# Kernel tuning notes

Measured on AMD Instinct MI355X. Metric: run time of the kernel, lower is better.

Reference implementation:

```python
import jax, jax.numpy as jnp
import numpy as np

N = 500000   # active voxels
CIN = 32
COUT = 64
K = 27       # 3x3x3 kernel taps
G = 8        # group norm groups
EPS = 1e-5


def group_norm(x, gamma, beta, num_groups=G, eps=EPS):
    # fvnn GroupNorm on sparse features with batch size 1: normalize each
    # channel-group over all active voxels (spatial) and channels in group.
    n, c = x.shape
    xg = x.reshape(n, num_groups, c // num_groups)
    mean = xg.mean(axis=(0, 2), keepdims=True)
    var = xg.var(axis=(0, 2), keepdims=True)
    xn = ((xg - mean) * jax.lax.rsqrt(var + eps)).reshape(n, c)
    return xn * gamma + beta


def sparse_conv(x, nbr_idx, W):
    # gather-based sparse 3x3x3 conv: W is [K, Cin, Cout]; loop over the 27
    # fixed kernel taps to avoid materializing the full [N, K, Cin] gather.
    out = jnp.zeros((x.shape[0], W.shape[2]), x.dtype)
    for k in range(W.shape[0]):
        out = out + jnp.take(x, nbr_idx[:, k], axis=0) @ W[k]
    return out


def setup_inputs() -> dict:
    key = jax.random.key(0)
    ks = jax.random.split(key, 8)
    s1 = 1.0 / np.sqrt(K * CIN)
    s2 = 1.0 / np.sqrt(K * COUT)
    return {
        "x": jax.random.normal(ks[0], (N, CIN), jnp.float32),
        "nbr_idx": jax.random.randint(ks[1], (N, K), 0, N, jnp.int32),
        "gamma1": jnp.ones((CIN,), jnp.float32),
        "beta1": jnp.zeros((CIN,), jnp.float32),
        "W1": jax.random.normal(ks[2], (K, CIN, COUT), jnp.float32) * s1,
        "gamma2": jnp.ones((COUT,), jnp.float32),
        "beta2": jnp.zeros((COUT,), jnp.float32),
        "W2": jax.random.normal(ks[3], (K, COUT, COUT), jnp.float32) * s2,
        "Wskip": jax.random.normal(ks[4], (CIN, COUT), jnp.float32) * (1.0 / np.sqrt(CIN)),
        "bskip": jnp.zeros((COUT,), jnp.float32),
        "feat_depth": 0,
    }


def reference(x, nbr_idx, gamma1, beta1, W1, gamma2, beta2, W2, Wskip, bskip, feat_depth):
    # decoder SparseResBlock, order 'gcs': GN -> SparseConv(bias=False) -> SiLU
    h = jax.nn.silu(sparse_conv(group_norm(x, gamma1, beta1), nbr_idx, W1))
    h = jax.nn.silu(sparse_conv(group_norm(h, gamma2, beta2), nbr_idx, W2))
    skip = x @ Wskip + bskip  # 1x1 sparse conv == per-voxel linear
    return (h + skip, feat_depth)
```

## Files before the change

kernel.cpp:

```cpp
#include <hip/hip_runtime.h>
#include <hip/hip_bf16.h>

typedef __bf16 bf16x8 __attribute__((ext_vector_type(8)));
typedef __bf16 bf16x4 __attribute__((ext_vector_type(4)));
typedef float  f32x4  __attribute__((ext_vector_type(4)));

#define MFMA16(a, b, c) __builtin_amdgcn_mfma_f32_16x16x32_bf16((a), (b), (c), 0, 0, 0)

__global__ void zero_stats_kernel(float* s) { s[threadIdx.x] = 0.0f; }

__global__ __launch_bounds__(256) void caststats_kernel(
    const float4* __restrict__ x, bf16x4* __restrict__ xb,
    float* __restrict__ stats, int nvec)
{
    int nth = gridDim.x * blockDim.x;
    int gt = blockIdx.x * blockDim.x + threadIdx.x;
    float s = 0.f, ss = 0.f;
    for (int f = gt; f < nvec; f += nth) {
        float4 v = x[f];
        s  += v.x + v.y + v.z + v.w;
        ss += v.x * v.x + v.y * v.y + v.z * v.z + v.w * v.w;
        bf16x4 b;
        b[0] = (__bf16)v.x; b[1] = (__bf16)v.y;
        b[2] = (__bf16)v.z; b[3] = (__bf16)v.w;
        xb[f] = b;
    }
    __shared__ float ls[16];
    if (threadIdx.x < 16) ls[threadIdx.x] = 0.f;
    __syncthreads();
    int g = gt & 7;
    atomicAdd(&ls[2 * g], s);
    atomicAdd(&ls[2 * g + 1], ss);
    __syncthreads();
    if (threadIdx.x < 16) atomicAdd(&stats[threadIdx.x], ls[threadIdx.x]);
}

__global__ __launch_bounds__(256) void fold1_kernel(
    const float* __restrict__ W1, const float* __restrict__ gamma1,
    const float* __restrict__ beta1, const float* __restrict__ Wskip,
    const float* __restrict__ stats1,
    __bf16* __restrict__ bp1, __bf16* __restrict__ bps,
    float* __restrict__ bias1,
    const int* __restrict__ feat, int* __restrict__ feat_out, float inv_n)
{
    int b = blockIdx.x, t = threadIdx.x;
    if (b < 216) {
        int e = b * 256 + t;
        int j = e & 7, lane = (e >> 3) & 63, ct = (e >> 9) & 3, k = e >> 11;
        int ci = ((lane >> 4) << 3) + j;
        int co = (ct << 4) + (lane & 15);
        int g = ci >> 2;
        float mean = stats1[2 * g] * inv_n;
        float var  = stats1[2 * g + 1] * inv_n - mean * mean;
        float r = rsqrtf(var + 1e-5f);
        float a = gamma1[ci] * r;
        bp1[e] = (__bf16)(a * W1[k * 2048 + ci * 64 + co]);
    } else if (b == 216) {
        if (t < 64) {
            float sum = 0.0f;
            for (int ci = 0; ci < 32; ++ci) {
                int g = ci >> 2;
                float mean = stats1[2 * g] * inv_n;
                float var  = stats1[2 * g + 1] * inv_n - mean * mean;
                float r = rsqrtf(var + 1e-5f);
                float a = gamma1[ci] * r;
                float bb = beta1[ci] - mean * a;
                float ws = 0.0f;
                for (int k = 0; k < 27; ++k) ws += W1[k * 2048 + ci * 64 + t];
                sum += bb * ws;
            }
            bias1[t] = sum;
        } else if (t == 64) {
            feat_out[0] = feat[0];
        }
    } else {
        int e = (b - 217) * 256 + t;
        int j = e & 7, lane = (e >> 3) & 63, ct = e >> 9;
        int ci = ((lane >> 4) << 3) + j;
        int co = (ct << 4) + (lane & 15);
        bps[e] = (__bf16)Wskip[ci * 64 + co];
    }
}

__global__ __launch_bounds__(256) void fold2_kernel(
    const float* __restrict__ W2, const float* __restrict__ gamma2,
    const float* __restrict__ beta2, const float* __restrict__ stats2,
    __bf16* __restrict__ bp2, float* __restrict__ bias2, float inv_n)
{
    int b = blockIdx.x, t = threadIdx.x;
    if (b < 432) {
        int e = b * 256 + t;
        int j = e & 7, lane = (e >> 3) & 63, ct = (e >> 9) & 3, hf = (e >> 11) & 1, k = e >> 12;
        int ci = (hf << 5) + ((lane >> 4) << 3) + j;
        int co = (ct << 4) + (lane & 15);
        int g = ci >> 3;
        float mean = stats2[2 * g] * inv_n;
        float var  = stats2[2 * g + 1] * inv_n - mean * mean;
        float r = rsqrtf(var + 1e-5f);
        float a = gamma2[ci] * r;
        bp2[e] = (__bf16)(a * W2[k * 4096 + ci * 64 + co]);
    } else if (t < 64) {
        float sum = 0.0f;
        for (int ci = 0; ci < 64; ++ci) {
            int g = ci >> 3;
            float mean = stats2[2 * g] * inv_n;
            float var  = stats2[2 * g + 1] * inv_n - mean * mean;
            float r = rsqrtf(var + 1e-5f);
            float a = gamma2[ci] * r;
            float bb = beta2[ci] - mean * a;
            float ws = 0.0f;
            for (int k = 0; k < 27; ++k) ws += W2[k * 4096 + ci * 64 + t];
            sum += bb * ws;
        }
        bias2[t] = sum;
    }
}

__global__ __launch_bounds__(256, 4) void conv1_kernel(
    const __bf16* __restrict__ xb, const int* __restrict__ nbr,
    const __bf16* __restrict__ bp1, const float* __restrict__ bias1,
    __bf16* __restrict__ h, float* __restrict__ stats2, int nTiles)
{
    __shared__ int sidx[4][864];
    __shared__ float ls[16];
    const int wav = threadIdx.x >> 6, lane = threadIdx.x & 63;
    const int unit = blockIdx.x * 4 + wav;
    const int t0 = unit * 2;
    const bool act0 = t0 < nTiles, act1 = t0 + 1 < nTiles;
    if (threadIdx.x < 16) ls[threadIdx.x] = 0.f;
    const int lm = lane & 15, q = lane >> 4;
    f32x4 c[8] = {};
    if (act0) {
        const int* gi = nbr + (size_t)t0 * 432;
        const int cnt = act1 ? 864 : 432;
        for (int i = lane; i < 864; i += 64) sidx[wav][i] = (i < cnt) ? gi[i] : 0;
        const int* s0p = &sidx[wav][lm * 27];
        const int* s1p = &sidx[wav][432 + lm * 27];
        const bf16x8* __restrict__ bpv = (const bf16x8*)bp1;
        bf16x8 a0 = *(const bf16x8*)(xb + (size_t)s0p[0] * 32 + q * 8);
        bf16x8 a1 = *(const bf16x8*)(xb + (size_t)s1p[0] * 32 + q * 8);
#pragma unroll
        for (int k = 0; k < 27; ++k) {
            bf16x8 n0 = a0, n1 = a1;
            if (k < 26) {
                n0 = *(const bf16x8*)(xb + (size_t)s0p[k + 1] * 32 + q * 8);
                n1 = *(const bf16x8*)(xb + (size_t)s1p[k + 1] * 32 + q * 8);
            }
            int bb = k * 256 + lane;
            bf16x8 b0 = bpv[bb], b1 = bpv[bb + 64], b2 = bpv[bb + 128], b3 = bpv[bb + 192];
            c[0] = MFMA16(a0, b0, c[0]);
            c[1] = MFMA16(a0, b1, c[1]);
            c[2] = MFMA16(a0, b2, c[2]);
            c[3] = MFMA16(a0, b3, c[3]);
            c[4] = MFMA16(a1, b0, c[4]);
            c[5] = MFMA16(a1, b1, c[5]);
            c[6] = MFMA16(a1, b2, c[6]);
            c[7] = MFMA16(a1, b3, c[7]);
            a0 = n0; a1 = n1;
        }
    }
    __syncthreads();
    if (act0) {
#define EPI1(CI, CT, V0) { \
        float bsv = bias1[(CT) * 16 + lm]; \
        float ps = 0.f, pss = 0.f; \
        _Pragma("unroll") \
        for (int r = 0; r < 4; ++r) { \
            float val = c[CI][r] + bsv; \
            val = val / (1.0f + __expf(-val)); \
            h[(size_t)((V0) + q * 4 + r) * 64 + (CT) * 16 + lm] = (__bf16)val; \
            ps += val; pss += val * val; } \
        int g2 = (CT) * 2 + (lm >> 3); \
        atomicAdd(&ls[2 * g2], ps); atomicAdd(&ls[2 * g2 + 1], pss); }
        const int v0 = t0 * 16;
        EPI1(0, 0, v0) EPI1(1, 1, v0) EPI1(2, 2, v0) EPI1(3, 3, v0)
        if (act1) {
            const int v1 = v0 + 16;
            EPI1(4, 0, v1) EPI1(5, 1, v1) EPI1(6, 2, v1) EPI1(7, 3, v1)
        }
#undef EPI1
    }
    __syncthreads();
    if (threadIdx.x < 16) atomicAdd(&stats2[threadIdx.x], ls[threadIdx.x]);
}

__global__ __launch_bounds__(256, 4) void conv2_kernel(
    const __bf16* __restrict__ h, const __bf16* __restrict__ xb,
    const int* __restrict__ nbr,
    const __bf16* __restrict__ bp2, const __bf16* __restrict__ bps,
    const float* __restrict__ bias2, const float* __restrict__ bskip,
    float* __restrict__ out, int nTiles)
{
    __shared__ int sidx[4][864];
    const int wav = threadIdx.x >> 6, lane = threadIdx.x & 63;
    const int unit = blockIdx.x * 4 + wav;
    const int t0 = unit * 2;
    const bool act0 = t0 < nTiles, act1 = t0 + 1 < nTiles;
    if (!act0) return;
    const int lm = lane & 15, q = lane >> 4;
    const int* gi = nbr + (size_t)t0 * 432;
    const int cnt = act1 ? 864 : 432;
    for (int i = lane; i < 864; i += 64) sidx[wav][i] = (i < cnt) ? gi[i] : 0;
    const int* s0p = &sidx[wav][lm * 27];
    const int* s1p = &sidx[wav][432 + lm * 27];
    const bf16x8* __restrict__ bpv = (const bf16x8*)bp2;
    const bf16x8* __restrict__ bsp = (const bf16x8*)bps;
    f32x4 c[8] = {};
    {
        const __bf16* r0 = h + (size_t)s0p[0] * 64;
        const __bf16* r1 = h + (size_t)s1p[0] * 64;
        bf16x8 a0l = *(const bf16x8*)(r0 + q * 8);
        bf16x8 a0h = *(const bf16x8*)(r0 + 32 + q * 8);
        bf16x8 a1l = *(const bf16x8*)(r1 + q * 8);
        bf16x8 a1h = *(const bf16x8*)(r1 + 32 + q * 8);
#pragma unroll
        for (int k = 0; k < 27; ++k) {
            bf16x8 n0l = a0l, n0h = a0h, n1l = a1l, n1h = a1h;
            if (k < 26) {
                const __bf16* p0 = h + (size_t)s0p[k + 1] * 64;
                const __bf16* p1 = h + (size_t)s1p[k + 1] * 64;
                n0l = *(const bf16x8*)(p0 + q * 8);
                n0h = *(const bf16x8*)(p0 + 32 + q * 8);
                n1l = *(const bf16x8*)(p1 + q * 8);
                n1h = *(const bf16x8*)(p1 + 32 + q * 8);
            }
            int bb = k * 512 + lane;
            bf16x8 b0 = bpv[bb],       b1 = bpv[bb + 64];
            bf16x8 b2 = bpv[bb + 128], b3 = bpv[bb + 192];
            c[0] = MFMA16(a0l, b0, c[0]);
            c[1] = MFMA16(a0l, b1, c[1]);
            c[2] = MFMA16(a0l, b2, c[2]);
            c[3] = MFMA16(a0l, b3, c[3]);
            c[4] = MFMA16(a1l, b0, c[4]);
            c[5] = MFMA16(a1l, b1, c[5]);
            c[6] = MFMA16(a1l, b2, c[6]);
            c[7] = MFMA16(a1l, b3, c[7]);
            bf16x8 b4 = bpv[bb + 256], b5 = bpv[bb + 320];
            bf16x8 b6 = bpv[bb + 384], b7 = bpv[bb + 448];
            c[0] = MFMA16(a0h, b4, c[0]);
            c[1] = MFMA16(a0h, b5, c[1]);
            c[2] = MFMA16(a0h, b6, c[2]);
            c[3] = MFMA16(a0h, b7, c[3]);
            c[4] = MFMA16(a1h, b4, c[4]);
            c[5] = MFMA16(a1h, b5, c[5]);
            c[6] = MFMA16(a1h, b6, c[6]);
            c[7] = MFMA16(a1h, b7, c[7]);
            a0l = n0l; a0h = n0h; a1l = n1l; a1h = n1h;
        }
    }
    f32x4 s[8] = {};
    {
        bf16x8 ax0 = *(const bf16x8*)(xb + ((size_t)t0 * 16 + lm) * 32 + q * 8);
        bf16x8 w0 = bsp[lane], w1 = bsp[64 + lane], w2 = bsp[128 + lane], w3 = bsp[192 + lane];
        s[0] = MFMA16(ax0, w0, s[0]);
        s[1] = MFMA16(ax0, w1, s[1]);
        s[2] = MFMA16(ax0, w2, s[2]);
        s[3] = MFMA16(ax0, w3, s[3]);
        if (act1) {
            bf16x8 ax1 = *(const bf16x8*)(xb + ((size_t)t0 * 16 + 16 + lm) * 32 + q * 8);
            s[4] = MFMA16(ax1, w0, s[4]);
            s[5] = MFMA16(ax1, w1, s[5]);
            s[6] = MFMA16(ax1, w2, s[6]);
            s[7] = MFMA16(ax1, w3, s[7]);
        }
    }
#define EPI2(CI, CT, V0) { \
        int co = (CT) * 16 + lm; \
        float b2v = bias2[co]; \
        float bsk = bskip[co]; \
        _Pragma("unroll") \
        for (int r = 0; r < 4; ++r) { \
            float val = c[CI][r] + b2v; \
            val = val / (1.0f + __expf(-val)); \
            val += s[CI][r] + bsk; \
            out[(size_t)((V0) + q * 4 + r) * 64 + co] = val; } }
    const int v0 = t0 * 16;
    EPI2(0, 0, v0) EPI2(1, 1, v0) EPI2(2, 2, v0) EPI2(3, 3, v0)
    if (act1) {
        const int v1 = v0 + 16;
        EPI2(4, 0, v1) EPI2(5, 1, v1) EPI2(6, 2, v1) EPI2(7, 3, v1)
    }
#undef EPI2
}

extern "C" void kernel_launch(void* const* d_in, const int* in_sizes, int n_in,
                              void* d_out, int out_size, void* d_ws, size_t ws_size,
                              hipStream_t stream)
{
    (void)n_in; (void)out_size; (void)ws_size;
    const float* x      = (const float*)d_in[0];
    const int*   nbr    = (const int*)d_in[1];
    const float* gamma1 = (const float*)d_in[2];
    const float* beta1  = (const float*)d_in[3];
    const float* W1     = (const float*)d_in[4];
    const float* gamma2 = (const float*)d_in[5];
    const float* beta2  = (const float*)d_in[6];
    const float* W2     = (const float*)d_in[7];
    const float* Wskip  = (const float*)d_in[8];
    const float* bskip  = (const float*)d_in[9];
    const int*   feat   = (const int*)d_in[10];
    const int N = in_sizes[0] / 32;

    char* ws = (char*)d_ws;
    float* stats1 = (float*)ws;
    float* stats2 = stats1 + 16;
    float* bias1  = stats1 + 32;
    float* bias2  = stats1 + 96;
    __bf16* bp1 = (__bf16*)(ws + (1 << 10));
    __bf16* bps = (__bf16*)(ws + (1 << 17));
    __bf16* bp2 = (__bf16*)(ws + 144 * 1024);
    __bf16* xb  = (__bf16*)(ws + (1 << 20));
    __bf16* h   = (__bf16*)(ws + (size_t)34 * (1 << 20));
    float* outb = (float*)d_out;

    const int nTiles = (N + 15) / 16;
    const int units = (nTiles + 1) / 2;
    const int convBlocks = (units + 3) / 4;

    hipLaunchKernelGGL(zero_stats_kernel, dim3(1), dim3(32), 0, stream, stats1);
    hipLaunchKernelGGL(caststats_kernel, dim3(2048), dim3(256), 0, stream,
                       (const float4*)x, (bf16x4*)xb, stats1, N * 8);
    hipLaunchKernelGGL(fold1_kernel, dim3(225), dim3(256), 0, stream,
                       W1, gamma1, beta1, Wskip, stats1, bp1, bps, bias1,
                       feat, (int*)(outb + (size_t)N * 64),
                       1.0f / (4.0f * (float)N));
    hipLaunchKernelGGL(conv1_kernel, dim3(convBlocks), dim3(256), 0, stream,
                       xb, nbr, bp1, bias1, h, stats2, nTiles);
    hipLaunchKernelGGL(fold2_kernel, dim3(433), dim3(256), 0, stream,
                       W2, gamma2, beta2, stats2, bp2, bias2,
                       1.0f / (8.0f * (float)N));
    hipLaunchKernelGGL(conv2_kernel, dim3(convBlocks), dim3(256), 0, stream,
                       h, xb, nbr, bp2, bps, bias2, bskip, outb, nTiles);
}
```

Before: 862.4 us.

## Stage conv weights in LDS via async global_load_lds and deepen gather prefetch

Both conv kernels now copy the weights for three taps at a time into shared memory with async global-to-LDS loads that all four waves of the block share, instead of each wave reading the weight fragments from global memory. Gather prefetch distance is raised to three taps in conv1 and two taps in conv2, held in small register rings. The aim is less redundant per-wave weight traffic through the cache. In exchange, each kernel adds a shared-memory buffer and two block barriers per three-tap chunk, which likely drain outstanding gather loads. Waves with no tile now stay alive to take part in the barriers.

After: 812.9 us. 1.06x faster.

```diff
diff --git a/kernel.cpp b/kernel.cpp
--- a/kernel.cpp
+++ b/kernel.cpp
@@ -6,6 +6,12 @@
 typedef float  f32x4  __attribute__((ext_vector_type(4)));
 
 #define MFMA16(a, b, c) __builtin_amdgcn_mfma_f32_16x16x32_bf16((a), (b), (c), 0, 0, 0)
+
+__device__ __forceinline__ void async_copy16(const void* g, void* l) {
+    __builtin_amdgcn_global_load_lds(
+        (const __attribute__((address_space(1))) void*)g,
+        (__attribute__((address_space(3))) void*)l, 16, 0, 0);
+}
 
 __global__ void zero_stats_kernel(float* s) { s[threadIdx.x] = 0.0f; }
 
@@ -122,6 +128,7 @@
     __bf16* __restrict__ h, float* __restrict__ stats2, int nTiles)
 {
     __shared__ int sidx[4][864];
+    __shared__ __align__(16) __bf16 Bs[3 * 2048];
     __shared__ float ls[16];
     const int wav = threadIdx.x >> 6, lane = threadIdx.x & 63;
     const int unit = blockIdx.x * 4 + wav;
@@ -129,37 +136,64 @@
     const bool act0 = t0 < nTiles, act1 = t0 + 1 < nTiles;
     if (threadIdx.x < 16) ls[threadIdx.x] = 0.f;
     const int lm = lane & 15, q = lane >> 4;
+
+    {
+        const int tc = act0 ? t0 : 0;
+        const int* gi = nbr + (size_t)tc * 432;
+        const int cnt = (act0 && act1) ? 864 : 432;
+        for (int i = lane; i < 864; i += 64) sidx[wav][i] = (i < cnt) ? gi[i] : 0;
+    }
+    const int* s0p = &sidx[wav][lm * 27];
+    const int* s1p = &sidx[wav][432 + lm * 27];
+
+#pragma unroll
+    for (int i = 0; i < 3; ++i) {
+        int part = wav * 3 + i;
+        async_copy16(bp1 + (size_t)part * 512 + lane * 8, &Bs[part * 512]);
+    }
+
     f32x4 c[8] = {};
-    if (act0) {
-        const int* gi = nbr + (size_t)t0 * 432;
-        const int cnt = act1 ? 864 : 432;
-        for (int i = lane; i < 864; i += 64) sidx[wav][i] = (i < cnt) ? gi[i] : 0;
-        const int* s0p = &sidx[wav][lm * 27];
-        const int* s1p = &sidx[wav][432 + lm * 27];
-        const bf16x8* __restrict__ bpv = (const bf16x8*)bp1;
-        bf16x8 a0 = *(const bf16x8*)(xb + (size_t)s0p[0] * 32 + q * 8);
-        bf16x8 a1 = *(const bf16x8*)(xb + (size_t)s1p[0] * 32 + q * 8);
-#pragma unroll
-        for (int k = 0; k < 27; ++k) {
-            bf16x8 n0 = a0, n1 = a1;
-            if (k < 26) {
-                n0 = *(const bf16x8*)(xb + (size_t)s0p[k + 1] * 32 + q * 8);
-                n1 = *(const bf16x8*)(xb + (size_t)s1p[k + 1] * 32 + q * 8);
+    bf16x8 P0[3], P1[3];
+#pragma unroll
+    for (int k = 0; k < 3; ++k) {
+        P0[k] = *(const bf16x8*)(xb + (size_t)s0p[k] * 32 + q * 8);
+        P1[k] = *(const bf16x8*)(xb + (size_t)s1p[k] * 32 + q * 8);
+    }
+    __syncthreads();
+
+    const bf16x8* Bv = (const bf16x8*)Bs;
+#pragma unroll
+    for (int k = 0; k < 27; ++k) {
+        const int sl = k % 3;
+        bf16x8 n0, n1;
+        if (k + 3 < 27) {
+            n0 = *(const bf16x8*)(xb + (size_t)s0p[k + 3] * 32 + q * 8);
+            n1 = *(const bf16x8*)(xb + (size_t)s1p[k + 3] * 32 + q * 8);
+        }
+        const int bb = sl * 256 + lane;
+        bf16x8 b0 = Bv[bb], b1 = Bv[bb + 64], b2 = Bv[bb + 128], b3 = Bv[bb + 192];
+        bf16x8 a0 = P0[sl], a1 = P1[sl];
+        c[0] = MFMA16(a0, b0, c[0]);
+        c[1] = MFMA16(a0, b1, c[1]);
+        c[2] = MFMA16(a0, b2, c[2]);
+        c[3] = MFMA16(a0, b3, c[3]);
+        c[4] = MFMA16(a1, b0, c[4]);
+        c[5] = MFMA16(a1, b1, c[5]);
+        c[6] = MFMA16(a1, b2, c[6]);
+        c[7] = MFMA16(a1, b3, c[7]);
+        if (k + 3 < 27) { P0[sl] = n0; P1[sl] = n1; }
+        if ((k % 3) == 2 && k < 26) {
+            __syncthreads();
+            const __bf16* gsrc = bp1 + (size_t)(k / 3 + 1) * 3 * 2048;
+#pragma unroll
+            for (int i = 0; i < 3; ++i) {
+                int part = wav * 3 + i;
+                async_copy16(gsrc + (size_t)part * 512 + lane * 8, &Bs[part * 512]);
             }
-            int bb = k * 256 + lane;
-            bf16x8 b0 = bpv[bb], b1 = bpv[bb + 64], b2 = bpv[bb + 128], b3 = bpv[bb + 192];
-            c[0] = MFMA16(a0, b0, c[0]);
-            c[1] = MFMA16(a0, b1, c[1]);
-            c[2] = MFMA16(a0, b2, c[2]);
-            c[3] = MFMA16(a0, b3, c[3]);
-            c[4] = MFMA16(a1, b0, c[4]);
-            c[5] = MFMA16(a1, b1, c[5]);
-            c[6] = MFMA16(a1, b2, c[6]);
-            c[7] = MFMA16(a1, b3, c[7]);
-            a0 = n0; a1 = n1;
-        }
-    }
-    __syncthreads();
+            __syncthreads();
+        }
+    }
+
     if (act0) {
 #define EPI1(CI, CT, V0) { \
         float bsv = bias1[(CT) * 16 + lm]; \
@@ -192,64 +226,93 @@
     float* __restrict__ out, int nTiles)
 {
     __shared__ int sidx[4][864];
+    __shared__ __align__(16) __bf16 Bs[3 * 4096];
     const int wav = threadIdx.x >> 6, lane = threadIdx.x & 63;
     const int unit = blockIdx.x * 4 + wav;
     const int t0 = unit * 2;
     const bool act0 = t0 < nTiles, act1 = t0 + 1 < nTiles;
-    if (!act0) return;
     const int lm = lane & 15, q = lane >> 4;
-    const int* gi = nbr + (size_t)t0 * 432;
-    const int cnt = act1 ? 864 : 432;
-    for (int i = lane; i < 864; i += 64) sidx[wav][i] = (i < cnt) ? gi[i] : 0;
+
+    {
+        const int tc = act0 ? t0 : 0;
+        const int* gi = nbr + (size_t)tc * 432;
+        const int cnt = (act0 && act1) ? 864 : 432;
+        for (int i = lane; i < 864; i += 64) sidx[wav][i] = (i < cnt) ? gi[i] : 0;
+    }
     const int* s0p = &sidx[wav][lm * 27];
     const int* s1p = &sidx[wav][432 + lm * 27];
-    const bf16x8* __restrict__ bpv = (const bf16x8*)bp2;
-    const bf16x8* __restrict__ bsp = (const bf16x8*)bps;
+
+#pragma unroll
+    for (int i = 0; i < 6; ++i) {
+        int part = wav * 6 + i;
+        async_copy16(bp2 + (size_t)part * 512 + lane * 8, &Bs[part * 512]);
+    }
+
     f32x4 c[8] = {};
-    {
-        const __bf16* r0 = h + (size_t)s0p[0] * 64;
-        const __bf16* r1 = h + (size_t)s1p[0] * 64;
-        bf16x8 a0l = *(const bf16x8*)(r0 + q * 8);
-        bf16x8 a0h = *(const bf16x8*)(r0 + 32 + q * 8);
-        bf16x8 a1l = *(const bf16x8*)(r1 + q * 8);
-        bf16x8 a1h = *(const bf16x8*)(r1 + 32 + q * 8);
-#pragma unroll
-        for (int k = 0; k < 27; ++k) {
-            bf16x8 n0l = a0l, n0h = a0h, n1l = a1l, n1h = a1h;
-            if (k < 26) {
-                const __bf16* p0 = h + (size_t)s0p[k + 1] * 64;
-                const __bf16* p1 = h + (size_t)s1p[k + 1] * 64;
-                n0l = *(const bf16x8*)(p0 + q * 8);
-                n0h = *(const bf16x8*)(p0 + 32 + q * 8);
-                n1l = *(const bf16x8*)(p1 + q * 8);
-                n1h = *(const bf16x8*)(p1 + 32 + q * 8);
+    bf16x8 P0l[2], P0h[2], P1l[2], P1h[2];
+#pragma unroll
+    for (int k = 0; k < 2; ++k) {
+        const __bf16* r0 = h + (size_t)s0p[k] * 64;
+        const __bf16* r1 = h + (size_t)s1p[k] * 64;
+        P0l[k] = *(const bf16x8*)(r0 + q * 8);
+        P0h[k] = *(const bf16x8*)(r0 + 32 + q * 8);
+        P1l[k] = *(const bf16x8*)(r1 + q * 8);
+        P1h[k] = *(const bf16x8*)(r1 + 32 + q * 8);
+    }
+    __syncthreads();
+
+    const bf16x8* Bv = (const bf16x8*)Bs;
+#pragma unroll
+    for (int k = 0; k < 27; ++k) {
+        const int sl = k & 1;
+        bf16x8 n0l, n0h, n1l, n1h;
+        if (k + 2 < 27) {
+            const __bf16* p0 = h + (size_t)s0p[k + 2] * 64;
+            const __bf16* p1 = h + (size_t)s1p[k + 2] * 64;
+            n0l = *(const bf16x8*)(p0 + q * 8);
+            n0h = *(const bf16x8*)(p0 + 32 + q * 8);
+            n1l = *(const bf16x8*)(p1 + q * 8);
+            n1h = *(const bf16x8*)(p1 + 32 + q * 8);
+        }
+        const int bb = (k % 3) * 512 + lane;
+        bf16x8 b0 = Bv[bb],       b1 = Bv[bb + 64];
+        bf16x8 b2 = Bv[bb + 128], b3 = Bv[bb + 192];
+        bf16x8 a0l = P0l[sl], a0h = P0h[sl], a1l = P1l[sl], a1h = P1h[sl];
+        c[0] = MFMA16(a0l, b0, c[0]);
+        c[1] = MFMA16(a0l, b1, c[1]);
+        c[2] = MFMA16(a0l, b2, c[2]);
+        c[3] = MFMA16(a0l, b3, c[3]);
+        c[4] = MFMA16(a1l, b0, c[4]);
+        c[5] = MFMA16(a1l, b1, c[5]);
+        c[6] = MFMA16(a1l, b2, c[6]);
+        c[7] = MFMA16(a1l, b3, c[7]);
+        bf16x8 b4 = Bv[bb + 256], b5 = Bv[bb + 320];
+        bf16x8 b6 = Bv[bb + 384], b7 = Bv[bb + 448];
+        c[0] = MFMA16(a0h, b4, c[0]);
+        c[1] = MFMA16(a0h, b5, c[1]);
+        c[2] = MFMA16(a0h, b6, c[2]);
+        c[3] = MFMA16(a0h, b7, c[3]);
+        c[4] = MFMA16(a1h, b4, c[4]);
+        c[5] = MFMA16(a1h, b5, c[5]);
+        c[6] = MFMA16(a1h, b6, c[6]);
+        c[7] = MFMA16(a1h, b7, c[7]);
+        if (k + 2 < 27) { P0l[sl] = n0l; P0h[sl] = n0h; P1l[sl] = n1l; P1h[sl] = n1h; }
+        if ((k % 3) == 2 && k < 26) {
+            __syncthreads();
+            const __bf16* gsrc = bp2 + (size_t)(k / 3 + 1) * 3 * 4096;
+#pragma unroll
+            for (int i = 0; i < 6; ++i) {
+                int part = wav * 6 + i;
+                async_copy16(gsrc + (size_t)part * 512 + lane * 8, &Bs[part * 512]);
             }
-            int bb = k * 512 + lane;
-            bf16x8 b0 = bpv[bb],       b1 = bpv[bb + 64];
-            bf16x8 b2 = bpv[bb + 128], b3 = bpv[bb + 192];
-            c[0] = MFMA16(a0l, b0, c[0]);
-            c[1] = MFMA16(a0l, b1, c[1]);
-            c[2] = MFMA16(a0l, b2, c[2]);
-            c[3] = MFMA16(a0l, b3, c[3]);
-            c[4] = MFMA16(a1l, b0, c[4]);
-            c[5] = MFMA16(a1l, b1, c[5]);
-            c[6] = MFMA16(a1l, b2, c[6]);
-            c[7] = MFMA16(a1l, b3, c[7]);
-            bf16x8 b4 = bpv[bb + 256], b5 = bpv[bb + 320];
-            bf16x8 b6 = bpv[bb + 384], b7 = bpv[bb + 448];
-            c[0] = MFMA16(a0h, b4, c[0]);
-            c[1] = MFMA16(a0h, b5, c[1]);
-            c[2] = MFMA16(a0h, b6, c[2]);
-            c[3] = MFMA16(a0h, b7, c[3]);
-            c[4] = MFMA16(a1h, b4, c[4]);
-            c[5] = MFMA16(a1h, b5, c[5]);
-            c[6] = MFMA16(a1h, b6, c[6]);
-            c[7] = MFMA16(a1h, b7, c[7]);
-            a0l = n0l; a0h = n0h; a1l = n1l; a1h = n1h;
-        }
-    }
+            __syncthreads();
+        }
+    }
+
+    if (!act0) return;
     f32x4 s[8] = {};
     {
+        const bf16x8* bsp = (const bf16x8*)bps;
         bf16x8 ax0 = *(const bf16x8*)(xb + ((size_t)t0 * 16 + lm) * 32 + q * 8);
         bf16x8 w0 = bsp[lane], w1 = bsp[64 + lane], w2 = bsp[128 + lane], w3 = bsp[192 + lane];
         s[0] = MFMA16(ax0, w0, s[0]);
```

## Stage conv weights in LDS via async copies and deepen gather prefetch

Applied to the files above, without the earlier changes.

Both sparse conv kernels now stream the folded weight chunks (three taps at a time) into double-buffered shared memory using global_load_lds async copies, synchronised with barriers and explicit waitcnts. The neighbor-row gathers are prefetched six taps ahead in registers instead of one. The aim is to stop each wave reloading weights from global/L2 every tap and to hide gather latency better. In exchange, conv2 drops to 2 blocks per CU, more registers are live, inactive waves must stay alive for the barriers, and block-wide barriers per chunk add sync cost.

Result: slower. 1.657 ms (+92.2%).

```diff
diff --git a/kernel.cpp b/kernel.cpp
--- a/kernel.cpp
+++ b/kernel.cpp
@@ -6,23 +6,30 @@
 typedef float  f32x4  __attribute__((ext_vector_type(4)));
 
 #define MFMA16(a, b, c) __builtin_amdgcn_mfma_f32_16x16x32_bf16((a), (b), (c), 0, 0, 0)
+#define SB() __builtin_amdgcn_sched_barrier(0)
+
+__device__ __forceinline__ void async_copy16(const void* g, void* l) {
+    __builtin_amdgcn_global_load_lds(
+        (const __attribute__((address_space(1))) void*)g,
+        (__attribute__((address_space(3))) void*)l, 16, 0, 0);
+}
 
 __global__ void zero_stats_kernel(float* s) { s[threadIdx.x] = 0.0f; }
 
 __global__ __launch_bounds__(256) void caststats_kernel(
-    const float4* __restrict__ x, bf16x4* __restrict__ xb,
+    const f32x4* __restrict__ x, bf16x4* __restrict__ xb,
     float* __restrict__ stats, int nvec)
 {
     int nth = gridDim.x * blockDim.x;
     int gt = blockIdx.x * blockDim.x + threadIdx.x;
     float s = 0.f, ss = 0.f;
     for (int f = gt; f < nvec; f += nth) {
-        float4 v = x[f];
-        s  += v.x + v.y + v.z + v.w;
-        ss += v.x * v.x + v.y * v.y + v.z * v.z + v.w * v.w;
+        f32x4 v = x[f];
+        s  += v[0] + v[1] + v[2] + v[3];
+        ss += v[0] * v[0] + v[1] * v[1] + v[2] * v[2] + v[3] * v[3];
         bf16x4 b;
-        b[0] = (__bf16)v.x; b[1] = (__bf16)v.y;
-        b[2] = (__bf16)v.z; b[3] = (__bf16)v.w;
+        b[0] = (__bf16)v[0]; b[1] = (__bf16)v[1];
+        b[2] = (__bf16)v[2]; b[3] = (__bf16)v[3];
         xb[f] = b;
     }
     __shared__ float ls[16];
@@ -122,6 +129,7 @@
     __bf16* __restrict__ h, float* __restrict__ stats2, int nTiles)
 {
     __shared__ int sidx[4][864];
+    __shared__ __align__(16) __bf16 Bs[2][3 * 2048];
     __shared__ float ls[16];
     const int wav = threadIdx.x >> 6, lane = threadIdx.x & 63;
     const int unit = blockIdx.x * 4 + wav;
@@ -129,37 +137,64 @@
     const bool act0 = t0 < nTiles, act1 = t0 + 1 < nTiles;
     if (threadIdx.x < 16) ls[threadIdx.x] = 0.f;
     const int lm = lane & 15, q = lane >> 4;
+
+    {
+        const int tc = act0 ? t0 : 0;
+        const int* gi = nbr + (size_t)tc * 432;
+        const int cnt = (act0 && act1) ? 864 : 432;
+        for (int i = lane; i < 864; i += 64) sidx[wav][i] = (i < cnt) ? gi[i] : 0;
+    }
+    const int* s0p = &sidx[wav][lm * 27];
+    const int* s1p = &sidx[wav][432 + lm * 27];
+    const bf16x8* Bv0 = (const bf16x8*)Bs[0];
+    const bf16x8* Bv1 = (const bf16x8*)Bs[1];
+
     f32x4 c[8] = {};
-    if (act0) {
-        const int* gi = nbr + (size_t)t0 * 432;
-        const int cnt = act1 ? 864 : 432;
-        for (int i = lane; i < 864; i += 64) sidx[wav][i] = (i < cnt) ? gi[i] : 0;
-        const int* s0p = &sidx[wav][lm * 27];
-        const int* s1p = &sidx[wav][432 + lm * 27];
-        const bf16x8* __restrict__ bpv = (const bf16x8*)bp1;
-        bf16x8 a0 = *(const bf16x8*)(xb + (size_t)s0p[0] * 32 + q * 8);
-        bf16x8 a1 = *(const bf16x8*)(xb + (size_t)s1p[0] * 32 + q * 8);
-#pragma unroll
-        for (int k = 0; k < 27; ++k) {
-            bf16x8 n0 = a0, n1 = a1;
-            if (k < 26) {
-                n0 = *(const bf16x8*)(xb + (size_t)s0p[k + 1] * 32 + q * 8);
-                n1 = *(const bf16x8*)(xb + (size_t)s1p[k + 1] * 32 + q * 8);
-            }
-            int bb = k * 256 + lane;
-            bf16x8 b0 = bpv[bb], b1 = bpv[bb + 64], b2 = bpv[bb + 128], b3 = bpv[bb + 192];
-            c[0] = MFMA16(a0, b0, c[0]);
-            c[1] = MFMA16(a0, b1, c[1]);
-            c[2] = MFMA16(a0, b2, c[2]);
-            c[3] = MFMA16(a0, b3, c[3]);
-            c[4] = MFMA16(a1, b0, c[4]);
-            c[5] = MFMA16(a1, b1, c[5]);
-            c[6] = MFMA16(a1, b2, c[6]);
-            c[7] = MFMA16(a1, b3, c[7]);
-            a0 = n0; a1 = n1;
-        }
-    }
-    __syncthreads();
+    bf16x8 P0[6], P1[6];
+
+#define STG1(CNK, BUF) { const __bf16* gs = bp1 + (size_t)(CNK) * 3 * 2048; \
+    _Pragma("unroll") for (int i = 0; i < 3; ++i) { int part = wav * 3 + i; \
+        async_copy16(gs + part * 512 + lane * 8, &Bs[BUF][part * 512]); } }
+#define GT1(T, S) { \
+    P0[S] = *(const bf16x8*)(xb + (size_t)s0p[T] * 32 + q * 8); \
+    P1[S] = *(const bf16x8*)(xb + (size_t)s1p[T] * 32 + q * 8); }
+#define TAP1(T, S, BSEL) { const bf16x8* Bv = (BSEL) ? Bv1 : Bv0; \
+    const int bb = ((T) % 3) * 256 + lane; \
+    bf16x8 b0 = Bv[bb], b1 = Bv[bb + 64], b2 = Bv[bb + 128], b3 = Bv[bb + 192]; \
+    c[0] = MFMA16(P0[S], b0, c[0]); c[1] = MFMA16(P0[S], b1, c[1]); \
+    c[2] = MFMA16(P0[S], b2, c[2]); c[3] = MFMA16(P0[S], b3, c[3]); \
+    c[4] = MFMA16(P1[S], b0, c[4]); c[5] = MFMA16(P1[S], b1, c[5]); \
+    c[6] = MFMA16(P1[S], b2, c[6]); c[7] = MFMA16(P1[S], b3, c[7]); }
+#define CHK1(C) { \
+    STG1((C) + 1, ((C) + 1) & 1); SB(); \
+    TAP1(3*(C)+0, (3*(C)+0) % 6, (C) & 1); \
+    TAP1(3*(C)+1, (3*(C)+1) % 6, (C) & 1); \
+    TAP1(3*(C)+2, (3*(C)+2) % 6, (C) & 1); \
+    GT1(3*(C)+6, (3*(C)+6) % 6); \
+    GT1(3*(C)+7, (3*(C)+7) % 6); \
+    GT1(3*(C)+8, (3*(C)+8) % 6); \
+    SB(); \
+    asm volatile("s_waitcnt vmcnt(6) lgkmcnt(0)" ::: "memory"); \
+    __builtin_amdgcn_s_barrier(); SB(); }
+
+    STG1(0, 0); SB();
+    GT1(0, 0) GT1(1, 1) GT1(2, 2) GT1(3, 3) GT1(4, 4) GT1(5, 5)
+    SB();
+    asm volatile("s_waitcnt vmcnt(12)" ::: "memory");
+    __builtin_amdgcn_s_barrier(); SB();
+
+    CHK1(0) CHK1(1) CHK1(2) CHK1(3) CHK1(4) CHK1(5) CHK1(6)
+    STG1(8, 0); SB();
+    TAP1(21, 3, 1) TAP1(22, 4, 1) TAP1(23, 5, 1)
+    SB();
+    asm volatile("s_waitcnt vmcnt(0) lgkmcnt(0)" ::: "memory");
+    __builtin_amdgcn_s_barrier(); SB();
+    TAP1(24, 0, 0) TAP1(25, 1, 0) TAP1(26, 2, 0)
+#undef CHK1
+#undef TAP1
+#undef GT1
+#undef STG1
+
     if (act0) {
 #define EPI1(CI, CT, V0) { \
         float bsv = bias1[(CT) * 16 + lm]; \
@@ -184,7 +219,7 @@
     if (threadIdx.x < 16) atomicAdd(&stats2[threadIdx.x], ls[threadIdx.x]);
 }
 
-__global__ __launch_bounds__(256, 4) void conv2_kernel(
+__global__ __launch_bounds__(256, 2) void conv2_kernel(
     const __bf16* __restrict__ h, const __bf16* __restrict__ xb,
     const int* __restrict__ nbr,
     const __bf16* __restrict__ bp2, const __bf16* __restrict__ bps,
@@ -192,64 +227,82 @@
     float* __restrict__ out, int nTiles)
 {
     __shared__ int sidx[4][864];
+    __shared__ __align__(16) __bf16 Bs[2][3 * 4096];
     const int wav = threadIdx.x >> 6, lane = threadIdx.x & 63;
     const int unit = blockIdx.x * 4 + wav;
     const int t0 = unit * 2;
     const bool act0 = t0 < nTiles, act1 = t0 + 1 < nTiles;
-    if (!act0) return;
     const int lm = lane & 15, q = lane >> 4;
-    const int* gi = nbr + (size_t)t0 * 432;
-    const int cnt = act1 ? 864 : 432;
-    for (int i = lane; i < 864; i += 64) sidx[wav][i] = (i < cnt) ? gi[i] : 0;
+
+    {
+        const int tc = act0 ? t0 : 0;
+        const int* gi = nbr + (size_t)tc * 432;
+        const int cnt = (act0 && act1) ? 864 : 432;
+        for (int i = lane; i < 864; i += 64) sidx[wav][i] = (i < cnt) ? gi[i] : 0;
+    }
     const int* s0p = &sidx[wav][lm * 27];
     const int* s1p = &sidx[wav][432 + lm * 27];
-    const bf16x8* __restrict__ bpv = (const bf16x8*)bp2;
-    const bf16x8* __restrict__ bsp = (const bf16x8*)bps;
+    const bf16x8* Bv0 = (const bf16x8*)Bs[0];
+    const bf16x8* Bv1 = (const bf16x8*)Bs[1];
+
     f32x4 c[8] = {};
-    {
-        const __bf16* r0 = h + (size_t)s0p[0] * 64;
-        const __bf16* r1 = h + (size_t)s1p[0] * 64;
-        bf16x8 a0l = *(const bf16x8*)(r0 + q * 8);
-        bf16x8 a0h = *(const bf16x8*)(r0 + 32 + q * 8);
-        bf16x8 a1l = *(const bf16x8*)(r1 + q * 8);
-        bf16x8 a1h = *(const bf16x8*)(r1 + 32 + q * 8);
-#pragma unroll
-        for (int k = 0; k < 27; ++k) {
-            bf16x8 n0l = a0l, n0h = a0h, n1l = a1l, n1h = a1h;
-            if (k < 26) {
-                const __bf16* p0 = h + (size_t)s0p[k + 1] * 64;
-                const __bf16* p1 = h + (size_t)s1p[k + 1] * 64;
-                n0l = *(const bf16x8*)(p0 + q * 8);
-                n0h = *(const bf16x8*)(p0 + 32 + q * 8);
-                n1l = *(const bf16x8*)(p1 + q * 8);
-                n1h = *(const bf16x8*)(p1 + 32 + q * 8);
-            }
-            int bb = k * 512 + lane;
-            bf16x8 b0 = bpv[bb],       b1 = bpv[bb + 64];
-            bf16x8 b2 = bpv[bb + 128], b3 = bpv[bb + 192];
-            c[0] = MFMA16(a0l, b0, c[0]);
-            c[1] = MFMA16(a0l, b1, c[1]);
-            c[2] = MFMA16(a0l, b2, c[2]);
-            c[3] = MFMA16(a0l, b3, c[3]);
-            c[4] = MFMA16(a1l, b0, c[4]);
-            c[5] = MFMA16(a1l, b1, c[5]);
-            c[6] = MFMA16(a1l, b2, c[6]);
-            c[7] = MFMA16(a1l, b3, c[7]);
-            bf16x8 b4 = bpv[bb + 256], b5 = bpv[bb + 320];
-            bf16x8 b6 = bpv[bb + 384], b7 = bpv[bb + 448];
-            c[0] = MFMA16(a0h, b4, c[0]);
-            c[1] = MFMA16(a0h, b5, c[1]);
-            c[2] = MFMA16(a0h, b6, c[2]);
-            c[3] = MFMA16(a0h, b7, c[3]);
-            c[4] = MFMA16(a1h, b4, c[4]);
-            c[5] = MFMA16(a1h, b5, c[5]);
-            c[6] = MFMA16(a1h, b6, c[6]);
-            c[7] = MFMA16(a1h, b7, c[7]);
-            a0l = n0l; a0h = n0h; a1l = n1l; a1h = n1h;
-        }
-    }
+    bf16x8 P0l[6], P0h[6], P1l[6], P1h[6];
+
+#define STG2(CNK, BUF) { const __bf16* gs = bp2 + (size_t)(CNK) * 3 * 4096; \
+    _Pragma("unroll") for (int i = 0; i < 6; ++i) { int part = wav * 6 + i; \
+        async_copy16(gs + part * 512 + lane * 8, &Bs[BUF][part * 512]); } }
+#define GT2(T, S) { const __bf16* p0 = h + (size_t)s0p[T] * 64; \
+    const __bf16* p1 = h + (size_t)s1p[T] * 64; \
+    P0l[S] = *(const bf16x8*)(p0 + q * 8); \
+    P0h[S] = *(const bf16x8*)(p0 + 32 + q * 8); \
+    P1l[S] = *(const bf16x8*)(p1 + q * 8); \
+    P1h[S] = *(const bf16x8*)(p1 + 32 + q * 8); }
+#define TAP2(T, S, BSEL) { const bf16x8* Bv = (BSEL) ? Bv1 : Bv0; \
+    const int bb = ((T) % 3) * 512 + lane; \
+    bf16x8 b0 = Bv[bb], b1 = Bv[bb + 64], b2 = Bv[bb + 128], b3 = Bv[bb + 192]; \
+    c[0] = MFMA16(P0l[S], b0, c[0]); c[1] = MFMA16(P0l[S], b1, c[1]); \
+    c[2] = MFMA16(P0l[S], b2, c[2]); c[3] = MFMA16(P0l[S], b3, c[3]); \
+    c[4] = MFMA16(P1l[S], b0, c[4]); c[5] = MFMA16(P1l[S], b1, c[5]); \
+    c[6] = MFMA16(P1l[S], b2, c[6]); c[7] = MFMA16(P1l[S], b3, c[7]); \
+    bf16x8 b4 = Bv[bb + 256], b5 = Bv[bb + 320], b6 = Bv[bb + 384], b7 = Bv[bb + 448]; \
+    c[0] = MFMA16(P0h[S], b4, c[0]); c[1] = MFMA16(P0h[S], b5, c[1]); \
+    c[2] = MFMA16(P0h[S], b6, c[2]); c[3] = MFMA16(P0h[S], b7, c[3]); \
+    c[4] = MFMA16(P1h[S], b4, c[4]); c[5] = MFMA16(P1h[S], b5, c[5]); \
+    c[6] = MFMA16(P1h[S], b6, c[6]); c[7] = MFMA16(P1h[S], b7, c[7]); }
+#define CHK2(C) { \
+    STG2((C) + 1, ((C) + 1) & 1); SB(); \
+    TAP2(3*(C)+0, (3*(C)+0) % 6, (C) & 1); \
+    TAP2(3*(C)+1, (3*(C)+1) % 6, (C) & 1); \
+    TAP2(3*(C)+2, (3*(C)+2) % 6, (C) & 1); \
+    GT2(3*(C)+6, (3*(C)+6) % 6); \
+    GT2(3*(C)+7, (3*(C)+7) % 6); \
+    GT2(3*(C)+8, (3*(C)+8) % 6); \
+    SB(); \
+    asm volatile("s_waitcnt vmcnt(12) lgkmcnt(0)" ::: "memory"); \
+    __builtin_amdgcn_s_barrier(); SB(); }
+
+    STG2(0, 0); SB();
+    GT2(0, 0) GT2(1, 1) GT2(2, 2) GT2(3, 3) GT2(4, 4) GT2(5, 5)
+    SB();
+    asm volatile("s_waitcnt vmcnt(24)" ::: "memory");
+    __builtin_amdgcn_s_barrier(); SB();
+
+    CHK2(0) CHK2(1) CHK2(2) CHK2(3) CHK2(4) CHK2(5) CHK2(6)
+    STG2(8, 0); SB();
+    TAP2(21, 3, 1) TAP2(22, 4, 1) TAP2(23, 5, 1)
+    SB();
+    asm volatile("s_waitcnt vmcnt(0) lgkmcnt(0)" ::: "memory");
+    __builtin_amdgcn_s_barrier(); SB();
+    TAP2(24, 0, 0) TAP2(25, 1, 0) TAP2(26, 2, 0)
+#undef CHK2
+#undef TAP2
+#undef GT2
+#undef STG2
+
+    if (!act0) return;
     f32x4 s[8] = {};
     {
+        const bf16x8* bsp = (const bf16x8*)bps;
         bf16x8 ax0 = *(const bf16x8*)(xb + ((size_t)t0 * 16 + lm) * 32 + q * 8);
         bf16x8 w0 = bsp[lane], w1 = bsp[64 + lane], w2 = bsp[128 + lane], w3 = bsp[192 + lane];
         s[0] = MFMA16(ax0, w0, s[0]);
@@ -319,7 +372,7 @@
 
     hipLaunchKernelGGL(zero_stats_kernel, dim3(1), dim3(32), 0, stream, stats1);
     hipLaunchKernelGGL(caststats_kernel, dim3(2048), dim3(256), 0, stream,
-                       (const float4*)x, (bf16x4*)xb, stats1, N * 8);
+                       (const f32x4*)x, (bf16x4*)xb, stats1, N * 8);
     hipLaunchKernelGGL(fold1_kernel, dim3(225), dim3(256), 0, stream,
                        W1, gamma1, beta1, Wskip, stats1, bp1, bps, bias1,
                        feat, (int*)(outb + (size_t)N * 64),
```
